# Kernel optimization log

Hardware: AMD Instinct MI355X
Metric: run time of the kernel (lower is better)

Reference implementation:

```python
import jax, jax.numpy as jnp
import numpy as np

B, C_IN, T, H, W = 32, 1024, 7, 14, 14
C_INTER = 512


def setup_inputs() -> dict:
    key = jax.random.key(0)
    ks = jax.random.split(key, 8)
    s = lambda fan_in: 1.0 / np.sqrt(fan_in)
    return {
        "x_window": jax.random.normal(ks[0], (B, C_IN, T, H, W), jnp.float32),
        "nodes": jax.random.normal(ks[1], (T, C_INTER), jnp.float32),
        "Wq": jax.random.normal(ks[2], (C_IN, C_INTER), jnp.float32) * s(C_IN),
        "bq": jnp.zeros((C_INTER,), jnp.float32),
        "Wk": jax.random.normal(ks[3], (C_INTER, C_INTER), jnp.float32) * s(C_INTER),
        "bk": jnp.zeros((C_INTER,), jnp.float32),
        "Wv": jax.random.normal(ks[4], (C_IN, C_INTER), jnp.float32) * s(C_IN),
        "bv": jnp.zeros((C_INTER,), jnp.float32),
        "Wo": jax.random.normal(ks[5], (C_INTER, C_IN), jnp.float32) * s(C_INTER),
        "bo": jnp.zeros((C_IN,), jnp.float32),
    }


def reference(x_window, nodes, Wq, bq, Wk, bk, Wv, bv, Wo, bo):
    # x_window: (B, C_in, T, H, W); dropout is identity at eval time.
    t_mid = x_window.shape[2] // 2
    x_item = x_window[:, :, t_mid]                                   # (B, C_in, H, W)
    # pointwise (Linear3d) projections over channel dim
    query = jnp.einsum("bchw,cd->bdhw", x_item, Wq) + bq[None, :, None, None]
    key = nodes @ Wk + bk                                            # (T, C_inter)
    value = jnp.einsum("bcthw,cd->bdthw", x_window, Wv) + bv[None, :, None, None, None]
    # per-pixel attention scores over the T node keys
    alpha = jnp.einsum("bdhw,td->bthw", query, key)                  # (B, T, H, W)
    alpha = jax.nn.softmax(alpha, axis=1)
    # per-pixel weighted temporal sum
    y = jnp.einsum("bthw,bdthw->bdhw", alpha, value)                 # (B, C_inter, H, W)
    out = jnp.einsum("bdhw,dc->bchw", y, Wo) + bo[None, :, None, None]
    return out[:, :, None]                                           # (B, C_in, 1, H, W)
```

## Files before the change

### kernel.cpp

```cpp
#include <hip/hip_runtime.h>
#include <hip/hip_bf16.h>
#include <stdint.h>

#define BB    32
#define CIN   1024
#define TT    7
#define HHWW  196
#define HW4   49
#define CI    512
#define TMID  3
#define MM    (BB*HHWW)

using bf16 = __hip_bfloat16;
typedef __attribute__((ext_vector_type(8))) short short8;
typedef __attribute__((ext_vector_type(4))) short s16x4;
typedef __attribute__((ext_vector_type(4))) float f32x4;

__device__ __forceinline__ void gload_lds16(const void* g, void* l) {
    __builtin_amdgcn_global_load_lds((const __attribute__((address_space(1))) void*)g,
                                     (__attribute__((address_space(3))) void*)l, 16, 0, 0);
}

template <int EPI>
__device__ __forceinline__ void gemm_body(const bf16* __restrict__ A, const bf16* __restrict__ Bt,
                                          void* __restrict__ Cout, const float* __restrict__ bias,
                                          int M, int N, int K, int bm, int bn,
                                          bf16 (&As)[128 * 64], bf16 (&Bs)[128 * 64]) {
    int tid = threadIdx.x;
    int wid = tid >> 6, lane = tid & 63;
    int wr = wid >> 1, wc = wid & 1;
    f32x4 acc[4][4] = {};
    const bf16* Ab = A + (size_t)bm * 128 * K;
    const bf16* Bb = Bt + (size_t)bn * 128 * K;
    int row = lane & 15;
    int kb_base = (lane >> 4) * 8;

    for (int k0 = 0; k0 < K; k0 += 64) {
        #pragma unroll
        for (int it = 0; it < 4; ++it) {
            int e = (it * 256 + tid) * 8;
            int r = e >> 6, cc = e & 63;
            gload_lds16(Ab + (size_t)r * K + k0 + cc, &As[e]);
            gload_lds16(Bb + (size_t)r * K + k0 + cc, &Bs[e]);
        }
        __syncthreads();
        #pragma unroll
        for (int kk = 0; kk < 2; ++kk) {
            int kb = kk * 32 + kb_base;
            short8 a[4], b[4];
            #pragma unroll
            for (int mi = 0; mi < 4; ++mi) a[mi] = *(const short8*)&As[(wr * 64 + mi * 16 + row) * 64 + kb];
            #pragma unroll
            for (int ni = 0; ni < 4; ++ni) b[ni] = *(const short8*)&Bs[(wc * 64 + ni * 16 + row) * 64 + kb];
            #pragma unroll
            for (int mi = 0; mi < 4; ++mi)
                #pragma unroll
                for (int ni = 0; ni < 4; ++ni)
                    acc[mi][ni] = __builtin_amdgcn_mfma_f32_16x16x32_bf16(a[mi], b[ni], acc[mi][ni], 0, 0, 0);
        }
        __syncthreads();
    }

    int col_l = lane & 15, row_l = (lane >> 4) * 4;
    if constexpr (EPI == 0) {
        bf16* C = (bf16*)Cout;
        #pragma unroll
        for (int mi = 0; mi < 4; ++mi) {
            int row0 = bm * 128 + wr * 64 + mi * 16 + row_l;
            #pragma unroll
            for (int ni = 0; ni < 4; ++ni) {
                int col = bn * 128 + wc * 64 + ni * 16 + col_l;
                #pragma unroll
                for (int r = 0; r < 4; ++r)
                    C[(size_t)(row0 + r) * N + col] = __float2bfloat16(acc[mi][ni][r]);
            }
        }
    } else {
        float* Cf = (float*)Cout;
        #pragma unroll
        for (int ni = 0; ni < 4; ++ni) {
            int n = bn * 128 + wc * 64 + ni * 16 + col_l;
            float bz = bias[n];
            #pragma unroll
            for (int mi = 0; mi < 4; ++mi) {
                int m0 = bm * 128 + wr * 64 + mi * 16 + row_l;
                int b = m0 / HHWW;
                int hw0 = m0 - b * HHWW;
                f32x4 v = acc[mi][ni];
                v[0] += bz; v[1] += bz; v[2] += bz; v[3] += bz;
                *(f32x4*)&Cf[((size_t)b * CIN + n) * HHWW + hw0] = v;
            }
        }
    }
}

__global__ __launch_bounds__(256) void k_prep1(
    const float* __restrict__ nodes, const float* __restrict__ Wk, const float* __restrict__ bk,
    float* __restrict__ key,
    const float* __restrict__ Wv, const float* __restrict__ Wo,
    bf16* __restrict__ Wv_bf, bf16* __restrict__ WoT_bf,
    const float* __restrict__ bv, const float* __restrict__ bo, float* __restrict__ bvo) {
    __shared__ float sred[512];
    int bid = blockIdx.x, tid = threadIdx.x;
    if (bid < 56) {
        int t = bid >> 3, dc = bid & 7;
        int d_l = tid & 63, q = tid >> 6;
        int d = dc * 64 + d_l;
        float acc = 0.f;
        const float* nr = nodes + t * CI;
        #pragma unroll 4
        for (int c = q * 128; c < q * 128 + 128; ++c)
            acc = fmaf(nr[c], Wk[(size_t)c * CI + d], acc);
        sred[q * 64 + d_l] = acc;
        __syncthreads();
        if (q == 0)
            key[t * CI + d] = sred[d_l] + sred[64 + d_l] + sred[128 + d_l] + sred[192 + d_l] + bk[d];
    } else if (bid < 56 + 2048) {
        int i = (bid - 56) * 256 + tid;
        Wv_bf[i] = __float2bfloat16(Wv[i]);
        int d = i >> 10, cp = i & 1023;
        WoT_bf[(size_t)cp * CI + d] = __float2bfloat16(Wo[i]);
    } else {
        int cp0 = (bid - 2104) * 32;
        int cp_l = tid & 31, dq = tid >> 5;
        float acc = 0.f;
        #pragma unroll 4
        for (int d = dq * 64; d < dq * 64 + 64; ++d)
            acc = fmaf(bv[d], Wo[(size_t)d * CIN + cp0 + cp_l], acc);
        sred[dq * 32 + cp_l] = acc;
        __syncthreads();
        if (dq == 0) {
            float v = bo[cp0 + cp_l];
            #pragma unroll
            for (int g = 0; g < 8; ++g) v += sred[g * 32 + cp_l];
            bvo[cp0 + cp_l] = v;
        }
    }
}

__global__ __launch_bounds__(256) void k_wqk(const float* __restrict__ Wq, const float* __restrict__ bq,
                                             const float* __restrict__ key, float* __restrict__ Wqk,
                                             float* __restrict__ bqk) {
    int c = blockIdx.x * 4 + (threadIdx.x >> 6);
    int lane = threadIdx.x & 63;
    if (c > CIN) return;
    const float* src = (c < CIN) ? (Wq + (size_t)c * CI) : bq;
    float acc[TT] = {};
    #pragma unroll 2
    for (int it = 0; it < CI / 64; ++it) {
        float w = src[it * 64 + lane];
        #pragma unroll
        for (int t = 0; t < TT; ++t) acc[t] = fmaf(w, key[t * CI + it * 64 + lane], acc[t]);
    }
    #pragma unroll
    for (int t = 0; t < TT; ++t) {
        float v = acc[t];
        for (int off = 32; off; off >>= 1) v += __shfl_down(v, off);
        if (lane == 0) { if (c < CIN) Wqk[c * 8 + t] = v; else bqk[t] = v; }
    }
}

__global__ __launch_bounds__(256) void k_prep3(
    const float* __restrict__ x, const float* __restrict__ Wqk, float* __restrict__ part,
    const bf16* __restrict__ WoT_bf, const bf16* __restrict__ Wv_bf, bf16* __restrict__ WvoT) {
    __shared__ __align__(16) bf16 As[128 * 64];
    __shared__ __align__(16) bf16 Bs[128 * 64];
    __shared__ float wq_s[128 * 8];
    int bid = blockIdx.x, tid = threadIdx.x;
    if (bid < 64) {
        gemm_body<0>(WoT_bf, Wv_bf, (void*)WvoT, nullptr, 1024, 1024, 512, bid >> 3, bid & 7, As, Bs);
        return;
    }
    int ab = bid - 64;
    int chunk = ab & 7, b = ab >> 3;
    for (int i = tid; i < 1024; i += 256) wq_s[i] = Wqk[chunk * 1024 + i];
    __syncthreads();
    if (tid < HHWW) {
        float acc[TT] = {};
        const float* xb = x + (size_t)(b * CIN + chunk * 128) * TT * HHWW + TMID * HHWW + tid;
        #pragma unroll 4
        for (int c = 0; c < 128; ++c) {
            float v = xb[(size_t)c * TT * HHWW];
            #pragma unroll
            for (int t = 0; t < TT; ++t) acc[t] = fmaf(v, wq_s[c * 8 + t], acc[t]);
        }
        #pragma unroll
        for (int t = 0; t < TT; ++t)
            part[((size_t)(b * 8 + chunk) * TT + t) * HHWW + tid] = acc[t];
    }
}

__global__ __launch_bounds__(256) void k_smxw(const float* __restrict__ x,
                                              const float* __restrict__ part,
                                              const float* __restrict__ bqk,
                                              bf16* __restrict__ xw) {
    __shared__ __align__(16) float al[TT * HHWW];
    __shared__ __align__(16) bf16 txp[HHWW * 32];
    int c0 = blockIdx.x * 32;
    int b = blockIdx.y;
    int tid = threadIdx.x;
    if (tid < HHWW) {
        float s[TT];
        #pragma unroll
        for (int t = 0; t < TT; ++t) s[t] = bqk[t];
        #pragma unroll
        for (int ch = 0; ch < 8; ++ch)
            #pragma unroll
            for (int t = 0; t < TT; ++t)
                s[t] += part[((size_t)(b * 8 + ch) * TT + t) * HHWW + tid];
        float mx = s[0];
        #pragma unroll
        for (int t = 1; t < TT; ++t) mx = fmaxf(mx, s[t]);
        float e[TT], sum = 0.f;
        #pragma unroll
        for (int t = 0; t < TT; ++t) { e[t] = __expf(s[t] - mx); sum += e[t]; }
        float inv = 1.f / sum;
        #pragma unroll
        for (int t = 0; t < TT; ++t) al[t * HHWW + tid] = e[t] * inv;
    }
    __syncthreads();
    const f32x4* xp = (const f32x4*)x;
    f32x4 acc[7] = {};
    #pragma unroll
    for (int t = 0; t < TT; ++t) {
        #pragma unroll
        for (int k = 0; k < 7; ++k) {
            int w = k * 256 + tid;
            if (k == 6 && w >= 1568) continue;
            int c_l = w / 49;
            int hw4 = w - c_l * 49;
            f32x4 a4 = *(const f32x4*)&al[t * HHWW + hw4 * 4];
            f32x4 xv = xp[((size_t)(b * CIN + c0 + c_l) * TT + t) * HW4 + hw4];
            acc[k] += a4 * xv;
        }
    }
    #pragma unroll
    for (int k = 0; k < 7; ++k) {
        int w = k * 256 + tid;
        if (k == 6 && w >= 1568) continue;
        int c_l = w / 49;
        int hw4 = w - c_l * 49;
        int v = (hw4 & 7) << 2;
        #pragma unroll
        for (int r = 0; r < 4; ++r)
            txp[(hw4 * 4 + r) * 32 + (c_l ^ v)] = __float2bfloat16(acc[k][r]);
    }
    __syncthreads();
    #pragma unroll
    for (int k = 0; k < 7; ++k) {
        int w = k * 256 + tid;
        if (k == 6 && w >= 1568) continue;
        int m = w >> 3, seg = w & 7;
        int v = ((m >> 2) & 7) << 2;
        s16x4 val = *(const s16x4*)&txp[m * 32 + ((seg * 4) ^ v)];
        *(s16x4*)&xw[(size_t)(b * HHWW + m) * CIN + c0 + seg * 4] = val;
    }
}

__global__ __launch_bounds__(256) void k_gemm1(const bf16* __restrict__ A, const bf16* __restrict__ Bt,
                                               float* __restrict__ C, const float* __restrict__ bias) {
    __shared__ __align__(16) bf16 As[128 * 64];
    __shared__ __align__(16) bf16 Bs[128 * 64];
    gemm_body<1>(A, Bt, (void*)C, bias, MM, CIN, CIN, blockIdx.x, blockIdx.y, As, Bs);
}

extern "C" void kernel_launch(void* const* d_in, const int* in_sizes, int n_in,
                              void* d_out, int out_size, void* d_ws, size_t ws_size,
                              hipStream_t stream) {
    const float* x     = (const float*)d_in[0];
    const float* nodes = (const float*)d_in[1];
    const float* Wq    = (const float*)d_in[2];
    const float* bq    = (const float*)d_in[3];
    const float* Wk    = (const float*)d_in[4];
    const float* bk    = (const float*)d_in[5];
    const float* Wv    = (const float*)d_in[6];
    const float* bv    = (const float*)d_in[7];
    const float* Wo    = (const float*)d_in[8];
    const float* bo    = (const float*)d_in[9];

    uint8_t* w = (uint8_t*)d_ws;
    size_t off = 0;
    auto alloc = [&](size_t bytes) -> void* {
        void* p = w + off;
        off = (off + bytes + 255) & ~(size_t)255;
        return p;
    };
    float* key    = (float*)alloc((size_t)TT * CI * 4);
    float* Wqk    = (float*)alloc((size_t)CIN * 8 * 4);
    float* bqk    = (float*)alloc(8 * 4);
    float* bvo    = (float*)alloc((size_t)CIN * 4);
    bf16*  Wv_bf  = (bf16*)alloc((size_t)CIN * CI * 2);
    bf16*  WoT_bf = (bf16*)alloc((size_t)CIN * CI * 2);
    bf16*  WvoT   = (bf16*)alloc((size_t)CIN * CIN * 2);
    float* part   = (float*)alloc((size_t)BB * 8 * TT * HHWW * 4);
    bf16*  xw     = (bf16*)alloc((size_t)MM * CIN * 2);
    (void)ws_size;

    k_prep1<<<2136, 256, 0, stream>>>(nodes, Wk, bk, key, Wv, Wo, Wv_bf, WoT_bf, bv, bo, bvo);
    k_wqk<<<257, 256, 0, stream>>>(Wq, bq, key, Wqk, bqk);
    k_prep3<<<320, 256, 0, stream>>>(x, Wqk, part, WoT_bf, Wv_bf, WvoT);
    k_smxw<<<dim3(32, BB), 256, 0, stream>>>(x, part, bqk, xw);
    k_gemm1<<<dim3(MM / 128, CIN / 128), 256, 0, stream>>>(xw, WvoT, (float*)d_out, bvo);
}
```

Measured before the change: 100.5 us.

## Regroup prep kernels, split alpha reduction finer, and swizzle GEMM block order

Moves the WvoT weight GEMM out of the alpha-partial kernel and into the Wq·key kernel, so the alpha kernel becomes a standalone grid with 16 channel chunks of 64 instead of 8 chunks of 128. This gives the alpha kernel more parallelism and shorter dependency chains, at the cost of twice as many partials for the softmax kernel to sum. The final GEMM switches to a 1D grid with a remapped block index, which changes which tiles run concurrently and may improve L2 reuse.

```diff
diff --git a/kernel.cpp b/kernel.cpp
--- a/kernel.cpp
+++ b/kernel.cpp
@@ -10,6 +10,8 @@
 #define CI    512
 #define TMID  3
 #define MM    (BB*HHWW)
+#define NCH   16
+#define CSZ   64
 
 using bf16 = __hip_bfloat16;
 typedef __attribute__((ext_vector_type(8))) short short8;
@@ -138,10 +140,18 @@
     }
 }
 
-__global__ __launch_bounds__(256) void k_wqk(const float* __restrict__ Wq, const float* __restrict__ bq,
-                                             const float* __restrict__ key, float* __restrict__ Wqk,
-                                             float* __restrict__ bqk) {
-    int c = blockIdx.x * 4 + (threadIdx.x >> 6);
+__global__ __launch_bounds__(256) void k_prep2(
+    const bf16* __restrict__ WoT_bf, const bf16* __restrict__ Wv_bf, bf16* __restrict__ WvoT,
+    const float* __restrict__ Wq, const float* __restrict__ bq,
+    const float* __restrict__ key, float* __restrict__ Wqk, float* __restrict__ bqk) {
+    __shared__ __align__(16) bf16 As[128 * 64];
+    __shared__ __align__(16) bf16 Bs[128 * 64];
+    int bid = blockIdx.x;
+    if (bid < 64) {
+        gemm_body<0>(WoT_bf, Wv_bf, (void*)WvoT, nullptr, 1024, 1024, 512, bid >> 3, bid & 7, As, Bs);
+        return;
+    }
+    int c = (bid - 64) * 4 + (threadIdx.x >> 6);
     int lane = threadIdx.x & 63;
     if (c > CIN) return;
     const float* src = (c < CIN) ? (Wq + (size_t)c * CI) : bq;
@@ -160,33 +170,26 @@
     }
 }
 
-__global__ __launch_bounds__(256) void k_prep3(
-    const float* __restrict__ x, const float* __restrict__ Wqk, float* __restrict__ part,
-    const bf16* __restrict__ WoT_bf, const bf16* __restrict__ Wv_bf, bf16* __restrict__ WvoT) {
-    __shared__ __align__(16) bf16 As[128 * 64];
-    __shared__ __align__(16) bf16 Bs[128 * 64];
-    __shared__ float wq_s[128 * 8];
-    int bid = blockIdx.x, tid = threadIdx.x;
-    if (bid < 64) {
-        gemm_body<0>(WoT_bf, Wv_bf, (void*)WvoT, nullptr, 1024, 1024, 512, bid >> 3, bid & 7, As, Bs);
-        return;
-    }
-    int ab = bid - 64;
-    int chunk = ab & 7, b = ab >> 3;
-    for (int i = tid; i < 1024; i += 256) wq_s[i] = Wqk[chunk * 1024 + i];
+__global__ __launch_bounds__(256) void k_alpha(const float* __restrict__ x,
+                                               const float* __restrict__ Wqk,
+                                               float* __restrict__ part) {
+    __shared__ float wq_s[CSZ * 8];
+    int ch = blockIdx.x, b = blockIdx.y;
+    int tid = threadIdx.x;
+    for (int i = tid; i < CSZ * 8; i += 256) wq_s[i] = Wqk[ch * CSZ * 8 + i];
     __syncthreads();
     if (tid < HHWW) {
         float acc[TT] = {};
-        const float* xb = x + (size_t)(b * CIN + chunk * 128) * TT * HHWW + TMID * HHWW + tid;
-        #pragma unroll 4
-        for (int c = 0; c < 128; ++c) {
+        const float* xb = x + (size_t)(b * CIN + ch * CSZ) * TT * HHWW + TMID * HHWW + tid;
+        #pragma unroll 8
+        for (int c = 0; c < CSZ; ++c) {
             float v = xb[(size_t)c * TT * HHWW];
             #pragma unroll
             for (int t = 0; t < TT; ++t) acc[t] = fmaf(v, wq_s[c * 8 + t], acc[t]);
         }
         #pragma unroll
         for (int t = 0; t < TT; ++t)
-            part[((size_t)(b * 8 + chunk) * TT + t) * HHWW + tid] = acc[t];
+            part[((size_t)(b * NCH + ch) * TT + t) * HHWW + tid] = acc[t];
     }
 }
 
@@ -204,10 +207,10 @@
         #pragma unroll
         for (int t = 0; t < TT; ++t) s[t] = bqk[t];
         #pragma unroll
-        for (int ch = 0; ch < 8; ++ch)
+        for (int ch = 0; ch < NCH; ++ch)
             #pragma unroll
             for (int t = 0; t < TT; ++t)
-                s[t] += part[((size_t)(b * 8 + ch) * TT + t) * HHWW + tid];
+                s[t] += part[((size_t)(b * NCH + ch) * TT + t) * HHWW + tid];
         float mx = s[0];
         #pragma unroll
         for (int t = 1; t < TT; ++t) mx = fmaxf(mx, s[t]);
@@ -261,7 +264,10 @@
                                                float* __restrict__ C, const float* __restrict__ bias) {
     __shared__ __align__(16) bf16 As[128 * 64];
     __shared__ __align__(16) bf16 Bs[128 * 64];
-    gemm_body<1>(A, Bt, (void*)C, bias, MM, CIN, CIN, blockIdx.x, blockIdx.y, As, Bs);
+    int id = blockIdx.x;
+    int w = (id & 7) * 49 + (id >> 3);
+    int bm = w >> 3, bn = w & 7;
+    gemm_body<1>(A, Bt, (void*)C, bias, MM, CIN, CIN, bm, bn, As, Bs);
 }
 
 extern "C" void kernel_launch(void* const* d_in, const int* in_sizes, int n_in,
@@ -292,13 +298,13 @@
     bf16*  Wv_bf  = (bf16*)alloc((size_t)CIN * CI * 2);
     bf16*  WoT_bf = (bf16*)alloc((size_t)CIN * CI * 2);
     bf16*  WvoT   = (bf16*)alloc((size_t)CIN * CIN * 2);
-    float* part   = (float*)alloc((size_t)BB * 8 * TT * HHWW * 4);
+    float* part   = (float*)alloc((size_t)BB * NCH * TT * HHWW * 4);
     bf16*  xw     = (bf16*)alloc((size_t)MM * CIN * 2);
     (void)ws_size;
 
     k_prep1<<<2136, 256, 0, stream>>>(nodes, Wk, bk, key, Wv, Wo, Wv_bf, WoT_bf, bv, bo, bvo);
-    k_wqk<<<257, 256, 0, stream>>>(Wq, bq, key, Wqk, bqk);
-    k_prep3<<<320, 256, 0, stream>>>(x, Wqk, part, WoT_bf, Wv_bf, WvoT);
+    k_prep2<<<321, 256, 0, stream>>>(WoT_bf, Wv_bf, WvoT, Wq, bq, key, Wqk, bqk);
+    k_alpha<<<dim3(NCH, BB), 256, 0, stream>>>(x, Wqk, part);
     k_smxw<<<dim3(32, BB), 256, 0, stream>>>(x, part, bqk, xw);
-    k_gemm1<<<dim3(MM / 128, CIN / 128), 256, 0, stream>>>(xw, WvoT, (float*)d_out, bvo);
-}
+    k_gemm1<<<392, 256, 0, stream>>>(xw, WvoT, (float*)d_out, bvo);
+}
```

Result: slower. 107.7 us (+7.2%).
